# Kernel tuning notes

Measured on AMD Instinct MI355X. Metric: run time of the kernel, lower is better.

The kernel has to match this reference:

```python
import jax, jax.numpy as jnp
import numpy as np

TOP_K = 2
SCALING = 16.0 / 8.0  # alpha / rank


def setup_inputs() -> dict:
    key = jax.random.key(0)
    ks = jax.random.split(key, 9)
    B, V, D, P = 32, 21, 512, 64
    IN, OUT, E, R, H = D * P, 96, 8, 8, 256
    return {
        "x": jax.random.normal(ks[0], (B, V, D, P), jnp.float32),
        "W_base": jax.random.normal(ks[1], (OUT, IN), jnp.float32) * (IN ** -0.5),
        "b_base": jax.random.normal(ks[2], (OUT,), jnp.float32) * 0.01,
        "W1": jax.random.normal(ks[3], (H, D), jnp.float32) * (D ** -0.5),
        "b1": jax.random.normal(ks[4], (H,), jnp.float32) * 0.01,
        "W2": jax.random.normal(ks[5], (E, H), jnp.float32) * (H ** -0.5),
        "b2": jax.random.normal(ks[6], (E,), jnp.float32) * 0.01,
        "lora_A": jax.random.normal(ks[7], (E, R, IN), jnp.float32) * (IN ** -0.5),
        "lora_B": jax.random.normal(ks[8], (E, OUT, R), jnp.float32) * (R ** -0.5),
    }


def reference(x, W_base, b_base, W1, b1, W2, b2, lora_A, lora_B):
    B, V, D, P = x.shape
    E = lora_A.shape[0]
    # FlattenHead: flatten last two dims, then linear (dropout is identity in eval)
    flat = x.reshape(B, V, D * P)                      # [B, V, IN]
    base_out = flat @ W_base.T + b_base                # [B, V, OUT]
    # Router: pool over n_vars then patch dim -> [B, D]
    pooled = x.mean(axis=1).mean(axis=-1)
    h = jax.nn.relu(pooled @ W1.T + b1)
    logits = h @ W2.T + b2                             # [B, E]
    probs = jax.nn.softmax(logits, axis=-1)
    topw, topi = jax.lax.top_k(probs, TOP_K)           # [B, K]
    topw = topw / jnp.clip(topw.sum(-1, keepdims=True), 1e-6)
    # All LoRA experts (matches original dense compute), then weighted combine
    temp = jnp.einsum("bvi,eri->ebvr", flat, lora_A)   # [E, B, V, R]
    delta = jnp.einsum("ebvr,eor->ebvo", temp, lora_B) * SCALING  # [E, B, V, OUT]
    # Scatter top-k weights into dense [B, E] then combine (top-k sparse combine)
    w_full = jnp.zeros((B, E), x.dtype).at[jnp.arange(B)[:, None], topi].add(topw)
    moe_delta = jnp.einsum("be,ebvo->bvo", w_full, delta)
    return base_out + moe_delta, probs
```

## Files before the change

### kernel.cpp

```cpp
#include <hip/hip_runtime.h>

#define B_DIM 32
#define V_DIM 21
#define D_DIM 512
#define P_DIM 64
#define M_TOTAL 672
#define K_TOTAL 32768
#define OUT_DIM 96
#define E_DIM 8
#define R_DIM 8
#define H_DIM 256
#define N_TOTAL 160
#define SCALING 2.0f

#define BM 64
#define BK 128
#define KSPLIT 32
#define K_PER_BLOCK (K_TOTAL / KSPLIT)
#define CHUNKS (K_PER_BLOCK / BK)
#define LDS_K (BK + 8)

typedef __attribute__((ext_vector_type(4))) float floatx4;
typedef __attribute__((ext_vector_type(8))) short short8;

__device__ __forceinline__ unsigned short f2bf(float f) {
  union { float f; unsigned int u; } v; v.f = f;
  unsigned int u = v.u + (0x7FFFu + ((v.u >> 16) & 1u));
  return (unsigned short)(u >> 16);
}

__global__ __launch_bounds__(256) void pool_kernel(const float* __restrict__ x,
                                                   float* __restrict__ pooled) {
  int wid = blockIdx.x * 4 + (threadIdx.x >> 6);
  int lane = threadIdx.x & 63;
  int b = wid >> 9;
  int d = wid & 511;
  const float* base = x + (((size_t)b * V_DIM) * D_DIM + d) * P_DIM + lane;
  float s = 0.0f;
  #pragma unroll
  for (int v = 0; v < V_DIM; ++v) s += base[(size_t)v * D_DIM * P_DIM];
  #pragma unroll
  for (int off = 32; off > 0; off >>= 1) s += __shfl_down(s, off, 64);
  if (lane == 0) pooled[wid] = s * (1.0f / (V_DIM * (float)P_DIM));
}

__global__ __launch_bounds__(256, 2)
void gemm_kernel(const float* __restrict__ x, const float* __restrict__ W_base,
                 const float* __restrict__ lora_A, float* __restrict__ S) {
  __shared__ short ldsA[BM * LDS_K];
  __shared__ short ldsW[N_TOTAL * LDS_K];
  const int tid = threadIdx.x;
  const int m0 = blockIdx.x * BM;
  const int kbase = blockIdx.y * K_PER_BLOCK;
  const int lane = tid & 63;
  const int wave = tid >> 6;
  const int quad = lane >> 4;
  const int l16 = lane & 15;

  floatx4 acc[10];
  #pragma unroll
  for (int i = 0; i < 10; ++i) acc[i] = (floatx4)(0.0f);

  for (int c = 0; c < CHUNKS; ++c) {
    const int kc = kbase + c * BK;
    __syncthreads();
    #pragma unroll
    for (int it = 0; it < 4; ++it) {
      int idx = it * 256 + tid;
      int row = idx >> 4;
      int g = idx & 15;
      int m = m0 + row;
      float vals[8];
      if (m < M_TOTAL) {
        const floatx4* s4 = (const floatx4*)(x + (size_t)m * K_TOTAL + kc + g * 8);
        floatx4 v0 = s4[0], v1 = s4[1];
        vals[0] = v0[0]; vals[1] = v0[1]; vals[2] = v0[2]; vals[3] = v0[3];
        vals[4] = v1[0]; vals[5] = v1[1]; vals[6] = v1[2]; vals[7] = v1[3];
      } else {
        #pragma unroll
        for (int j = 0; j < 8; ++j) vals[j] = 0.0f;
      }
      short8 sv;
      #pragma unroll
      for (int j = 0; j < 8; ++j) sv[j] = (short)f2bf(vals[j]);
      *(short8*)&ldsA[row * LDS_K + g * 8] = sv;
    }
    #pragma unroll
    for (int it = 0; it < 10; ++it) {
      int idx = it * 256 + tid;
      int row = idx >> 4;
      int g = idx & 15;
      const float* rowp = (row < OUT_DIM) ? (W_base + (size_t)row * K_TOTAL)
                                          : (lora_A + (size_t)(row - OUT_DIM) * K_TOTAL);
      const floatx4* s4 = (const floatx4*)(rowp + kc + g * 8);
      floatx4 v0 = s4[0], v1 = s4[1];
      short8 sv;
      sv[0] = (short)f2bf(v0[0]); sv[1] = (short)f2bf(v0[1]);
      sv[2] = (short)f2bf(v0[2]); sv[3] = (short)f2bf(v0[3]);
      sv[4] = (short)f2bf(v1[0]); sv[5] = (short)f2bf(v1[1]);
      sv[6] = (short)f2bf(v1[2]); sv[7] = (short)f2bf(v1[3]);
      *(short8*)&ldsW[row * LDS_K + g * 8] = sv;
    }
    __syncthreads();
    #pragma unroll
    for (int ks = 0; ks < 4; ++ks) {
      const int ko = ks * 32 + quad * 8;
      short8 a = *(const short8*)&ldsA[(wave * 16 + l16) * LDS_K + ko];
      #pragma unroll
      for (int nt = 0; nt < 10; ++nt) {
        short8 b = *(const short8*)&ldsW[(nt * 16 + l16) * LDS_K + ko];
        acc[nt] = __builtin_amdgcn_mfma_f32_16x16x32_bf16(a, b, acc[nt], 0, 0, 0);
      }
    }
  }
  #pragma unroll
  for (int nt = 0; nt < 10; ++nt) {
    #pragma unroll
    for (int r = 0; r < 4; ++r) {
      int m = m0 + wave * 16 + quad * 4 + r;
      int n = nt * 16 + l16;
      if (m < M_TOTAL) atomicAdd(&S[(size_t)m * N_TOTAL + n], acc[nt][r]);
    }
  }
}

__global__ __launch_bounds__(256)
void router_kernel(const float* __restrict__ pooled, const float* __restrict__ W1,
                   const float* __restrict__ b1, const float* __restrict__ W2,
                   const float* __restrict__ b2, float* __restrict__ wfull,
                   float* __restrict__ probs_out) {
  __shared__ float sp[D_DIM];
  __shared__ float sh[H_DIM];
  __shared__ float slog[E_DIM];
  const int b = blockIdx.x;
  const int t = threadIdx.x;
  sp[t] = pooled[b * D_DIM + t];
  sp[t + 256] = pooled[b * D_DIM + t + 256];
  __syncthreads();
  float acc = b1[t];
  const float* w1r = W1 + (size_t)t * D_DIM;
  for (int d = 0; d < D_DIM; ++d) acc += sp[d] * w1r[d];
  sh[t] = fmaxf(acc, 0.0f);
  __syncthreads();
  if (t < E_DIM) {
    float a = b2[t];
    const float* w2r = W2 + t * H_DIM;
    for (int j = 0; j < H_DIM; ++j) a += sh[j] * w2r[j];
    slog[t] = a;
  }
  __syncthreads();
  if (t == 0) {
    float p[E_DIM];
    float mx = slog[0];
    for (int e = 1; e < E_DIM; ++e) mx = fmaxf(mx, slog[e]);
    float se = 0.0f;
    for (int e = 0; e < E_DIM; ++e) { p[e] = __expf(slog[e] - mx); se += p[e]; }
    float inv = 1.0f / se;
    for (int e = 0; e < E_DIM; ++e) { p[e] *= inv; probs_out[b * E_DIM + e] = p[e]; }
    int i0 = 0;
    for (int e = 1; e < E_DIM; ++e) if (p[e] > p[i0]) i0 = e;
    int i1 = (i0 == 0) ? 1 : 0;
    for (int e = 0; e < E_DIM; ++e) if (e != i0 && p[e] > p[i1]) i1 = e;
    float s2 = p[i0] + p[i1];
    float invs = 1.0f / fmaxf(s2, 1e-6f);
    for (int e = 0; e < E_DIM; ++e) {
      float w = 0.0f;
      if (e == i0) w += p[i0] * invs;
      if (e == i1) w += p[i1] * invs;
      wfull[b * E_DIM + e] = w;
    }
  }
}

__global__ __launch_bounds__(256)
void combine_kernel(const float* __restrict__ S, const float* __restrict__ b_base,
                    const float* __restrict__ lora_B, const float* __restrict__ wfull,
                    float* __restrict__ out) {
  int idx = blockIdx.x * 256 + threadIdx.x;
  if (idx >= M_TOTAL * OUT_DIM) return;
  int bv = idx / OUT_DIM;
  int o = idx - bv * OUT_DIM;
  int b = bv / V_DIM;
  const float* srow = S + (size_t)bv * N_TOTAL;
  float base = srow[o] + b_base[o];
  float moe = 0.0f;
  #pragma unroll
  for (int e = 0; e < E_DIM; ++e) {
    float we = wfull[b * E_DIM + e];
    if (we != 0.0f) {
      const float* lb = lora_B + ((size_t)e * OUT_DIM + o) * R_DIM;
      const float* tr = srow + OUT_DIM + e * R_DIM;
      float d = 0.0f;
      #pragma unroll
      for (int r = 0; r < R_DIM; ++r) d += tr[r] * lb[r];
      moe += we * d;
    }
  }
  out[idx] = base + SCALING * moe;
}

extern "C" void kernel_launch(void* const* d_in, const int* in_sizes, int n_in,
                              void* d_out, int out_size, void* d_ws, size_t ws_size,
                              hipStream_t stream) {
  const float* x      = (const float*)d_in[0];
  const float* W_base = (const float*)d_in[1];
  const float* b_base = (const float*)d_in[2];
  const float* W1     = (const float*)d_in[3];
  const float* b1     = (const float*)d_in[4];
  const float* W2     = (const float*)d_in[5];
  const float* b2     = (const float*)d_in[6];
  const float* lora_A = (const float*)d_in[7];
  const float* lora_B = (const float*)d_in[8];
  float* out = (float*)d_out;

  float* ws     = (float*)d_ws;
  float* pooled = ws;
  float* S      = ws + 16384;
  float* wfull  = ws + 16384 + (size_t)M_TOTAL * N_TOTAL;

  hipMemsetAsync(d_ws, 0, (16384 + (size_t)M_TOTAL * N_TOTAL) * sizeof(float), stream);

  pool_kernel<<<4096, 256, 0, stream>>>(x, pooled);
  gemm_kernel<<<dim3(11, KSPLIT), 256, 0, stream>>>(x, W_base, lora_A, S);
  router_kernel<<<B_DIM, 256, 0, stream>>>(pooled, W1, b1, W2, b2, wfull,
                                           out + (size_t)M_TOTAL * OUT_DIM);
  combine_kernel<<<(M_TOTAL * OUT_DIM + 255) / 256, 256, 0, stream>>>(
      S, b_base, lora_B, wfull, out);
}
```

Before: 223.7 us.

## Fuse router pooling into the GEMM's x-tile load path

Removes the separate pooling kernel and computes the per-(batch, d) means inside the GEMM while it already loads x tiles. Partial sums go into LDS with shared-memory atomics and are then atomically added to the global pooled buffer. This avoids a second full read of x and one kernel launch, at the cost of extra LDS atomics in the GEMM load loop.

```diff
diff --git a/kernel.cpp b/kernel.cpp
--- a/kernel.cpp
+++ b/kernel.cpp
@@ -12,6 +12,7 @@
 #define H_DIM 256
 #define N_TOTAL 160
 #define SCALING 2.0f
+#define POOL_SCALE (1.0f / (V_DIM * (float)P_DIM))
 
 #define BM 64
 #define BK 128
@@ -29,26 +30,13 @@
   return (unsigned short)(u >> 16);
 }
 
-__global__ __launch_bounds__(256) void pool_kernel(const float* __restrict__ x,
-                                                   float* __restrict__ pooled) {
-  int wid = blockIdx.x * 4 + (threadIdx.x >> 6);
-  int lane = threadIdx.x & 63;
-  int b = wid >> 9;
-  int d = wid & 511;
-  const float* base = x + (((size_t)b * V_DIM) * D_DIM + d) * P_DIM + lane;
-  float s = 0.0f;
-  #pragma unroll
-  for (int v = 0; v < V_DIM; ++v) s += base[(size_t)v * D_DIM * P_DIM];
-  #pragma unroll
-  for (int off = 32; off > 0; off >>= 1) s += __shfl_down(s, off, 64);
-  if (lane == 0) pooled[wid] = s * (1.0f / (V_DIM * (float)P_DIM));
-}
-
 __global__ __launch_bounds__(256, 2)
 void gemm_kernel(const float* __restrict__ x, const float* __restrict__ W_base,
-                 const float* __restrict__ lora_A, float* __restrict__ S) {
+                 const float* __restrict__ lora_A, float* __restrict__ S,
+                 float* __restrict__ pooled) {
   __shared__ short ldsA[BM * LDS_K];
   __shared__ short ldsW[N_TOTAL * LDS_K];
+  __shared__ float lds_pool[5 * 16];
   const int tid = threadIdx.x;
   const int m0 = blockIdx.x * BM;
   const int kbase = blockIdx.y * K_PER_BLOCK;
@@ -56,6 +44,10 @@
   const int wave = tid >> 6;
   const int quad = lane >> 4;
   const int l16 = lane & 15;
+  const int b_first = m0 / V_DIM;
+  const int d_first = kbase >> 6;
+
+  if (tid < 80) lds_pool[tid] = 0.0f;
 
   floatx4 acc[10];
   #pragma unroll
@@ -76,6 +68,11 @@
         floatx4 v0 = s4[0], v1 = s4[1];
         vals[0] = v0[0]; vals[1] = v0[1]; vals[2] = v0[2]; vals[3] = v0[3];
         vals[4] = v1[0]; vals[5] = v1[1]; vals[6] = v1[2]; vals[7] = v1[3];
+        float sum8 = (vals[0] + vals[1]) + (vals[2] + vals[3]) +
+                     ((vals[4] + vals[5]) + (vals[6] + vals[7]));
+        int b_local = (m / V_DIM) - b_first;
+        int d_local = ((kc + g * 8) >> 6) - d_first;
+        atomicAdd(&lds_pool[b_local * 16 + d_local], sum8);
       } else {
         #pragma unroll
         for (int j = 0; j < 8; ++j) vals[j] = 0.0f;
@@ -121,6 +118,12 @@
       int n = nt * 16 + l16;
       if (m < M_TOTAL) atomicAdd(&S[(size_t)m * N_TOTAL + n], acc[nt][r]);
     }
+  }
+  if (tid < 80) {
+    int b = b_first + (tid >> 4);
+    int d = d_first + (tid & 15);
+    if (b < B_DIM)
+      atomicAdd(&pooled[b * D_DIM + d], lds_pool[tid] * POOL_SCALE);
   }
 }
 
@@ -220,8 +223,7 @@
 
   hipMemsetAsync(d_ws, 0, (16384 + (size_t)M_TOTAL * N_TOTAL) * sizeof(float), stream);
 
-  pool_kernel<<<4096, 256, 0, stream>>>(x, pooled);
-  gemm_kernel<<<dim3(11, KSPLIT), 256, 0, stream>>>(x, W_base, lora_A, S);
+  gemm_kernel<<<dim3(11, KSPLIT), 256, 0, stream>>>(x, W_base, lora_A, S, pooled);
   router_kernel<<<B_DIM, 256, 0, stream>>>(pooled, W1, b1, W2, b2, wfull,
                                            out + (size_t)M_TOTAL * OUT_DIM);
   combine_kernel<<<(M_TOTAL * OUT_DIM + 255) / 256, 256, 0, stream>>>(
```

After: 220.0 us. No clear change (-1.7%).
